# Kernel optimization log

Measured on AMD Instinct MI355X. Metric: run time of the kernel, lower is better.

The kernel has to match this reference:

```python
import jax, jax.numpy as jnp
import numpy as np

B, LT, D, N, H = 16, 512, 1024, 4096, 16
LN_EPS = 1e-5


def setup_inputs() -> dict:
    key = jax.random.key(0)
    ks = jax.random.split(key, 10)
    s = 0.02
    struct_token = jax.random.normal(ks[0], (N, D), dtype=jnp.float32)
    text_token = jax.random.normal(ks[1], (B, LT, D), dtype=jnp.float32)
    # contiguous, sorted segment ids: 256 struct tokens per batch element
    struct_batch = jnp.repeat(jnp.arange(B, dtype=jnp.int32), N // B)
    return {
        "struct_token": struct_token,
        "text_token": text_token,
        "in_proj_w": jax.random.normal(ks[2], (3 * D, D), dtype=jnp.float32) * s,
        "in_proj_b": jnp.zeros((3 * D,), jnp.float32),
        "attn_out_w": jax.random.normal(ks[3], (D, D), dtype=jnp.float32) * s,
        "attn_out_b": jnp.zeros((D,), jnp.float32),
        "ln_g": jnp.ones((D,), jnp.float32),
        "ln_b": jnp.zeros((D,), jnp.float32),
        "proj_w": jax.random.normal(ks[4], (D, D), dtype=jnp.float32) * s,
        "proj_b": jnp.zeros((D,), jnp.float32),
        "struct_batch": struct_batch,
        "L_max": N // B,
    }


def reference(struct_token, text_token, in_proj_w, in_proj_b, attn_out_w,
              attn_out_b, ln_g, ln_b, proj_w, proj_b, struct_batch, L_max):
    Bq = text_token.shape[0]
    Dm = struct_token.shape[-1]
    dh = Dm // H
    Ntok = struct_token.shape[0]

    # ---- ragged pad-pack (struct_batch is sorted/contiguous per segment) ----
    counts = jnp.bincount(struct_batch, length=Bq)                 # [B]
    starts = jnp.concatenate([jnp.zeros((1,), counts.dtype),
                              jnp.cumsum(counts)[:-1]])            # [B]
    pos = jnp.arange(Ntok) - starts[struct_batch]                  # [N] position in segment
    padded = jnp.zeros((Bq, L_max, Dm), struct_token.dtype)
    padded = padded.at[struct_batch, pos].set(struct_token)        # [B, Ls, D]

    # ---- nn.MultiheadAttention (batch_first): Q=padded, K=V=text ----
    wq, wk, wv = in_proj_w[:Dm], in_proj_w[Dm:2 * Dm], in_proj_w[2 * Dm:]
    bq, bk, bv = in_proj_b[:Dm], in_proj_b[Dm:2 * Dm], in_proj_b[2 * Dm:]
    q = (padded @ wq.T + bq).reshape(Bq, L_max, H, dh)
    k = (text_token @ wk.T + bk).reshape(Bq, -1, H, dh)
    v = (text_token @ wv.T + bv).reshape(Bq, -1, H, dh)
    scores = jnp.einsum('bqhd,bkhd->bhqk', q, k) / jnp.sqrt(jnp.float32(dh))
    attn = jax.nn.softmax(scores, axis=-1)
    ctx = jnp.einsum('bhqk,bkhd->bqhd', attn, v).reshape(Bq, L_max, Dm)
    fused = ctx @ attn_out_w.T + attn_out_b                        # [B, Ls, D]

    # ---- LayerNorm + output projection ----
    mu = fused.mean(-1, keepdims=True)
    var = fused.var(-1, keepdims=True)
    fused = (fused - mu) * jax.lax.rsqrt(var + LN_EPS) * ln_g + ln_b
    fused = fused @ proj_w.T + proj_b

    # ---- unpack valid tokens + scatter-mean over segments ----
    tok = fused[struct_batch, pos]                                 # [N, D]
    seg_sum = jax.ops.segment_sum(tok, struct_batch, num_segments=Bq)
    return seg_sum / jnp.maximum(counts, 1)[:, None].astype(seg_sum.dtype)
```

## Files before the change

kernel.cpp:

```cpp
#include <hip/hip_runtime.h>

constexpr int B  = 16;
constexpr int LT = 512;
constexpr int D  = 1024;
constexpr int N  = 4096;
constexpr int H  = 16;
constexpr int DH = D / H;
constexpr int LMAX = N / B;
constexpr float LN_EPS = 1e-5f;

typedef short  s16x8 __attribute__((ext_vector_type(8)));
typedef float  f32x4 __attribute__((ext_vector_type(4)));

__device__ __forceinline__ unsigned short f2bf(float x) {
    unsigned int u = __float_as_uint(x);
    unsigned int r = (u + 0x7fffu + ((u >> 16) & 1u)) >> 16;
    return (unsigned short)r;
}
__device__ __forceinline__ float bf2f(unsigned short u) {
    return __uint_as_float((unsigned int)u << 16);
}

__device__ __forceinline__ void load_lds16(const void* g, void* l) {
    __builtin_amdgcn_global_load_lds(
        (const __attribute__((address_space(1))) unsigned int*)g,
        (__attribute__((address_space(3))) unsigned int*)l, 16, 0, 0);
}

__global__ __launch_bounds__(256) void cast3_prep(
        const float* __restrict__ x0, unsigned short* __restrict__ y0, int n0,
        const float* __restrict__ x1, unsigned short* __restrict__ y1, int n1,
        const float* __restrict__ x2, unsigned short* __restrict__ y2, int n2,
        const int* __restrict__ sb, int* __restrict__ counts, int* __restrict__ starts) {
    __shared__ int s_counts[B];
    int t = threadIdx.x;
    if (blockIdx.x == 6144) {
        if (t < B) s_counts[t] = 0;
        __syncthreads();
        for (int i = t; i < N; i += 256) atomicAdd(&s_counts[sb[i]], 1);
        __syncthreads();
        if (t == 0) {
            int run = 0;
            for (int b = 0; b < B; b++) { starts[b] = run; run += s_counts[b]; }
        }
        if (t < B) counts[t] = s_counts[t];
        return;
    }
    long long i = (long long)(blockIdx.x * 256 + t) * 8;
    const float* x; unsigned short* y;
    if (i < n0)                { x = x0 + i; y = y0 + i; }
    else if (i < (long long)n0 + n1) { long long j = i - n0; x = x1 + j; y = y1 + j; }
    else if (i < (long long)n0 + n1 + n2) { long long j = i - n0 - n1; x = x2 + j; y = y2 + j; }
    else return;
    float4 a = *(const float4*)x;
    float4 b = *(const float4*)(x + 4);
    ushort4 o1, o2;
    o1.x = f2bf(a.x); o1.y = f2bf(a.y); o1.z = f2bf(a.z); o1.w = f2bf(a.w);
    o2.x = f2bf(b.x); o2.y = f2bf(b.y); o2.z = f2bf(b.z); o2.w = f2bf(b.w);
    *(ushort4*)y = o1;
    *(ushort4*)(y + 4) = o2;
}

__global__ void scatter_full(const float* __restrict__ st,
                             const int* __restrict__ counts,
                             const int* __restrict__ starts,
                             unsigned short* __restrict__ padded) {
    int p = blockIdx.x, b = blockIdx.y;
    int d = threadIdx.x * 4;
    size_t off = ((size_t)(b * LMAX + p)) * D + d;
    ushort4 o = {0, 0, 0, 0};
    if (p < counts[b]) {
        float4 v = *(const float4*)&st[(size_t)(starts[b] + p) * D + d];
        o.x = f2bf(v.x); o.y = f2bf(v.y); o.z = f2bf(v.z); o.w = f2bf(v.w);
    }
    *(ushort4*)&padded[off] = o;
}

template<typename Epi>
__device__ __forceinline__ void gemm256x128(const unsigned short* __restrict__ A,
                                            const unsigned short* __restrict__ W,
                                            int K, int kbeg, int kend, int m0, int n0,
                                            unsigned short* __restrict__ As,
                                            unsigned short* __restrict__ Bs,
                                            Epi&& epi) {
    const int tid  = threadIdx.x;
    const int lane = tid & 63;
    const int wid  = tid >> 6;
    const int wr   = wid >> 2;
    const int wc   = wid & 3;
    const int fm   = lane & 15;
    const int quad = lane >> 4;

    const int NK = (kend - kbeg) >> 6;

    f32x4 acc[8][2];
#pragma unroll
    for (int i = 0; i < 8; i++)
#pragma unroll
        for (int j = 0; j < 2; j++) acc[i][j] = (f32x4){0.f, 0.f, 0.f, 0.f};

    auto stage = [&](int s) {
        const int k0  = kbeg + (s << 6);
        const int buf = s - (s / 3) * 3;
        unsigned short* Ad = As + buf * 16384;
        unsigned short* Bd = Bs + buf * 8192;
#pragma unroll
        for (int r = 0; r < 4; r++) {
            int ci  = r * 512 + tid;
            int row = ci >> 3;
            int sg  = (ci & 7) ^ (row & 7);
            load_lds16(A + (size_t)(m0 + row) * K + k0 + sg * 8, Ad + ci * 8);
        }
#pragma unroll
        for (int r = 0; r < 2; r++) {
            int ci  = r * 512 + tid;
            int row = ci >> 3;
            int sg  = (ci & 7) ^ (row & 7);
            load_lds16(W + (size_t)(n0 + row) * K + k0 + sg * 8, Bd + ci * 8);
        }
    };

    stage(0);
    stage(1);

    for (int s = 0; s < NK; s++) {
        if (s + 1 < NK) asm volatile("s_waitcnt vmcnt(6)" ::: "memory");
        else            asm volatile("s_waitcnt vmcnt(0)" ::: "memory");
        __builtin_amdgcn_s_barrier();
        __builtin_amdgcn_sched_barrier(0);

        if (s + 2 < NK) stage(s + 2);

        const int buf = s - (s / 3) * 3;
        const unsigned short* Ab = As + buf * 16384;
        const unsigned short* Bb = Bs + buf * 8192;

        s16x8 bfr[2][2];
#pragma unroll
        for (int j = 0; j < 2; j++) {
            int row = wc * 32 + j * 16 + fm;
#pragma unroll
            for (int kk = 0; kk < 2; kk++) {
                int sl = (kk * 4 + quad) ^ (row & 7);
                bfr[j][kk] = *(const s16x8*)&Bb[row * 64 + sl * 8];
            }
        }

        s16x8 afr[4][2];
#pragma unroll
        for (int i = 0; i < 4; i++) {
            int row = wr * 128 + i * 16 + fm;
#pragma unroll
            for (int kk = 0; kk < 2; kk++) {
                int sl = (kk * 4 + quad) ^ (row & 7);
                afr[i][kk] = *(const s16x8*)&Ab[row * 64 + sl * 8];
            }
        }
        __builtin_amdgcn_s_setprio(1);
#pragma unroll
        for (int kk = 0; kk < 2; kk++)
#pragma unroll
            for (int i = 0; i < 4; i++)
#pragma unroll
                for (int j = 0; j < 2; j++)
                    acc[i][j] = __builtin_amdgcn_mfma_f32_16x16x32_bf16(afr[i][kk], bfr[j][kk], acc[i][j], 0, 0, 0);
        __builtin_amdgcn_s_setprio(0);

#pragma unroll
        for (int i = 0; i < 4; i++) {
            int row = wr * 128 + 64 + i * 16 + fm;
#pragma unroll
            for (int kk = 0; kk < 2; kk++) {
                int sl = (kk * 4 + quad) ^ (row & 7);
                afr[i][kk] = *(const s16x8*)&Ab[row * 64 + sl * 8];
            }
        }
        __builtin_amdgcn_s_setprio(1);
#pragma unroll
        for (int kk = 0; kk < 2; kk++)
#pragma unroll
            for (int i = 0; i < 4; i++)
#pragma unroll
                for (int j = 0; j < 2; j++)
                    acc[4 + i][j] = __builtin_amdgcn_mfma_f32_16x16x32_bf16(afr[i][kk], bfr[j][kk], acc[4 + i][j], 0, 0, 0);
        __builtin_amdgcn_s_setprio(0);
    }

    const int fr = quad * 4;
#pragma unroll
    for (int h = 0; h < 2; h++)
#pragma unroll
        for (int i = 0; i < 4; i++)
#pragma unroll
            for (int j = 0; j < 2; j++) {
                int row = m0 + wr * 128 + h * 64 + i * 16 + fr;
                int col = n0 + wc * 32 + j * 16 + fm;
#pragma unroll
                for (int r = 0; r < 4; r++)
                    epi(row + r, col, acc[h * 4 + i][j][r]);
            }
}

__global__ __launch_bounds__(512, 2) void qkv_fused(const unsigned short* __restrict__ padded,
                                                    const unsigned short* __restrict__ text,
                                                    const unsigned short* __restrict__ wqkv,
                                                    const float* __restrict__ bqkv,
                                                    unsigned short* __restrict__ qpack,
                                                    unsigned short* __restrict__ kpack,
                                                    unsigned short* __restrict__ vpack) {
    __shared__ __align__(16) unsigned short As[3 * 16384];
    __shared__ __align__(16) unsigned short Bs[3 * 8192];
    int orig = blockIdx.x;
    int id = (orig & 7) * 80 + (orig >> 3);
    if (id < 128) {
        int mt = id >> 3, nt = id & 7;
        gemm256x128(padded, wqkv, D, 0, D, mt * 256, nt * 128, As, Bs,
            [&](int mm, int col, float v) {
                float val = v + bqkv[col];
                int b = mm >> 8, q = mm & 255;
                int h = col >> 6, d = col & 63;
                qpack[(size_t)(b * H + h) * 16384 + (d >> 3) * 2048 + q * 8 + (d & 7)] = f2bf(val);
            });
    } else if (id < 384) {
        int f = id - 128;
        int mt = f >> 3, nt = f & 7;
        gemm256x128(text, wqkv + (size_t)D * D, D, 0, D, mt * 256, nt * 128, As, Bs,
            [&](int mm, int col, float v) {
                float val = v + bqkv[D + col];
                int b = mm >> 9, key = mm & 511;
                int h = col >> 6, d = col & 63;
                kpack[(size_t)(b * H + h) * 32768 + (d >> 3) * 4096 + key * 8 + (d & 7)] = f2bf(val);
            });
    } else {
        int f = id - 384;
        int mt = f >> 6, nt = f & 63;
        gemm256x128(wqkv + 2 * (size_t)D * D, text, D, 0, D, mt * 256, nt * 128, As, Bs,
            [&](int mm, int col, float v) {
                float val = v + bqkv[2 * D + mm];
                int h = mm >> 6, d = mm & 63;
                int b = col >> 9, key = col & 511;
                vpack[(size_t)(b * H + h) * 32768 + (key >> 3) * 512 + d * 8 + (key & 7)] = f2bf(val);
            });
    }
}

__global__ __launch_bounds__(512, 2) void gemm_bf2(const unsigned short* __restrict__ A,
                                                   const unsigned short* __restrict__ W,
                                                   unsigned short* __restrict__ C0,
                                                   unsigned short* __restrict__ C1,
                                                   int Nn, int K) {
    __shared__ __align__(16) unsigned short As[3 * 16384];
    __shared__ __align__(16) unsigned short Bs[3 * 8192];
    int orig = blockIdx.x;
    int id = (orig & 7) * 32 + (orig >> 3);
    int kh = id >> 7;
    int f  = id & 127;
    int mt = f >> 3, nt = f & 7;
    unsigned short* C = kh ? C1 : C0;
    gemm256x128(A, W, K, kh * 512, (kh + 1) * 512, mt * 256, nt * 128, As, Bs,
        [&](int mm, int col, float v) {
            C[(size_t)mm * Nn + col] = f2bf(v);
        });
}

constexpr int PKW = 72;

__global__ __launch_bounds__(512) void attn_mfma(const unsigned short* __restrict__ qpack,
                                                 const unsigned short* __restrict__ kpack,
                                                 const unsigned short* __restrict__ vpack,
                                                 unsigned short* __restrict__ ctx) {
    __shared__ __align__(16) unsigned short KV[16384];
    __shared__ __align__(16) unsigned short Ps[8 * 16 * PKW];

    const int tid = threadIdx.x;
    const int lane = tid & 63;
    const int wv = tid >> 6;
    const int fm = lane & 15;
    const int quad = lane >> 4;
    const int h = blockIdx.x, b = blockIdx.y, half = blockIdx.z;
    const int q0 = half * 128 + wv * 16;

    const unsigned short* qp = qpack + (size_t)(b * H + h) * 16384;
    const unsigned short* kp = kpack + (size_t)(b * H + h) * 32768;
    const unsigned short* vp = vpack + (size_t)(b * H + h) * 32768;

    const s16x8 aq0 = *(const s16x8*)&qp[quad * 2048 + (q0 + fm) * 8];
    const s16x8 aq1 = *(const s16x8*)&qp[(4 + quad) * 2048 + (q0 + fm) * 8];

    f32x4 sc[32];

    for (int kc = 0; kc < 2; kc++) {
        __syncthreads();
#pragma unroll
        for (int it = 0; it < 4; it++) {
            int f = it * 512 + tid;
            load_lds16(kp + (f >> 8) * 4096 + kc * 2048 + (f & 255) * 8, KV + f * 8);
        }
        __syncthreads();
#pragma unroll
        for (int t = 0; t < 16; t++) {
            s16x8 bk0 = *(const s16x8*)&KV[quad * 2048 + (t * 16 + fm) * 8];
            s16x8 bk1 = *(const s16x8*)&KV[(4 + quad) * 2048 + (t * 16 + fm) * 8];
            f32x4 a = (f32x4){0.f, 0.f, 0.f, 0.f};
            a = __builtin_amdgcn_mfma_f32_16x16x32_bf16(aq0, bk0, a, 0, 0, 0);
            a = __builtin_amdgcn_mfma_f32_16x16x32_bf16(aq1, bk1, a, 0, 0, 0);
            sc[kc * 16 + t] = a;
        }
    }

    const float scale = 0.125f;
    float mx[4], l[4], inv[4];
#pragma unroll
    for (int r = 0; r < 4; r++) {
        float m = sc[0][r];
#pragma unroll
        for (int t = 1; t < 32; t++) m = fmaxf(m, sc[t][r]);
        mx[r] = m;
    }
#pragma unroll
    for (int o = 1; o < 16; o <<= 1)
#pragma unroll
        for (int r = 0; r < 4; r++) mx[r] = fmaxf(mx[r], __shfl_xor(mx[r], o));
#pragma unroll
    for (int r = 0; r < 4; r++) l[r] = 0.f;
#pragma unroll
    for (int t = 0; t < 32; t++)
#pragma unroll
        for (int r = 0; r < 4; r++) {
            float e = __expf((sc[t][r] - mx[r]) * scale);
            sc[t][r] = e;
            l[r] += e;
        }
#pragma unroll
    for (int o = 1; o < 16; o <<= 1)
#pragma unroll
        for (int r = 0; r < 4; r++) l[r] += __shfl_xor(l[r], o);
#pragma unroll
    for (int r = 0; r < 4; r++) inv[r] = 1.f / l[r];

    f32x4 co[4];
#pragma unroll
    for (int n = 0; n < 4; n++) co[n] = (f32x4){0.f, 0.f, 0.f, 0.f};
    unsigned short* Pw = Ps + wv * (16 * PKW);

    for (int vc = 0; vc < 2; vc++) {
        __syncthreads();
#pragma unroll
        for (int it = 0; it < 4; it++) {
            int f = it * 512 + tid;
            load_lds16(vp + vc * 16384 + f * 8, KV + f * 8);
        }
        __syncthreads();
        for (int cs = 0; cs < 4; cs++) {
            int c = vc * 4 + cs;
#pragma unroll
            for (int tt = 0; tt < 4; tt++)
#pragma unroll
                for (int r = 0; r < 4; r++)
                    Pw[(quad * 4 + r) * PKW + tt * 16 + fm] = f2bf(sc[c * 4 + tt][r]);
#pragma unroll
            for (int s = 0; s < 2; s++) {
                s16x8 ap = *(const s16x8*)&Pw[fm * PKW + s * 32 + quad * 8];
#pragma unroll
                for (int n = 0; n < 4; n++) {
                    s16x8 bv = *(const s16x8*)&KV[(cs * 8 + s * 4 + quad) * 512 + (n * 16 + fm) * 8];
                    co[n] = __builtin_amdgcn_mfma_f32_16x16x32_bf16(ap, bv, co[n], 0, 0, 0);
                }
            }
        }
    }

    const size_t obase = (size_t)(b * LMAX + q0) * D + h * DH;
#pragma unroll
    for (int n = 0; n < 4; n++)
#pragma unroll
        for (int r = 0; r < 4; r++)
            ctx[obase + (size_t)(quad * 4 + r) * D + n * 16 + fm] = f2bf(co[n][r] * inv[r]);
}

__global__ __launch_bounds__(256) void lnmean_kernel(const unsigned short* __restrict__ f1a,
                                                     const unsigned short* __restrict__ f1b,
                                                     const float* __restrict__ bo,
                                                     const float* __restrict__ g,
                                                     const float* __restrict__ bb,
                                                     const int* __restrict__ counts,
                                                     float* __restrict__ msum) {
    int b = blockIdx.x;
    int t = threadIdx.x;
    int wv = t >> 6, lane = t & 63;
    int cnt = counts[b];
    int s0 = blockIdx.y * 32 + wv * 8;
    int s1 = min(cnt, s0 + 8);

    float4 gg[4], bv[4], bo4[4];
#pragma unroll
    for (int c = 0; c < 4; c++) {
        gg[c]  = *(const float4*)&g[c * 256 + lane * 4];
        bv[c]  = *(const float4*)&bb[c * 256 + lane * 4];
        bo4[c] = *(const float4*)&bo[c * 256 + lane * 4];
    }
    float4 acc[4];
#pragma unroll
    for (int c = 0; c < 4; c++) acc[c] = (float4){0.f, 0.f, 0.f, 0.f};

    for (int s = s0; s < s1; s++) {
        size_t rbase = ((size_t)(b * LMAX + s)) * D;
        float4 v[4];
        float sm = 0.f, ss = 0.f;
#pragma unroll
        for (int c = 0; c < 4; c++) {
            ushort4 ua = *(const ushort4*)&f1a[rbase + c * 256 + lane * 4];
            ushort4 ub = *(const ushort4*)&f1b[rbase + c * 256 + lane * 4];
            v[c].x = bf2f(ua.x) + bf2f(ub.x) + bo4[c].x;
            v[c].y = bf2f(ua.y) + bf2f(ub.y) + bo4[c].y;
            v[c].z = bf2f(ua.z) + bf2f(ub.z) + bo4[c].z;
            v[c].w = bf2f(ua.w) + bf2f(ub.w) + bo4[c].w;
            sm += v[c].x + v[c].y + v[c].z + v[c].w;
            ss += v[c].x * v[c].x + v[c].y * v[c].y + v[c].z * v[c].z + v[c].w * v[c].w;
        }
#pragma unroll
        for (int o = 32; o; o >>= 1) { sm += __shfl_xor(sm, o); ss += __shfl_xor(ss, o); }
        float mu = sm * (1.f / D);
        float var = ss * (1.f / D) - mu * mu;
        float r = rsqrtf(var + LN_EPS);
#pragma unroll
        for (int c = 0; c < 4; c++) {
            acc[c].x += (v[c].x - mu) * r * gg[c].x + bv[c].x;
            acc[c].y += (v[c].y - mu) * r * gg[c].y + bv[c].y;
            acc[c].z += (v[c].z - mu) * r * gg[c].z + bv[c].z;
            acc[c].w += (v[c].w - mu) * r * gg[c].w + bv[c].w;
        }
    }
    float inv = 1.f / (float)max(cnt, 1);
#pragma unroll
    for (int c = 0; c < 4; c++) {
        int base = b * D + c * 256 + lane * 4;
        atomicAdd(&msum[base + 0], acc[c].x * inv);
        atomicAdd(&msum[base + 1], acc[c].y * inv);
        atomicAdd(&msum[base + 2], acc[c].z * inv);
        atomicAdd(&msum[base + 3], acc[c].w * inv);
    }
}

__global__ __launch_bounds__(256) void tproj_kernel(const float* __restrict__ msum,
                                                    const float* __restrict__ W,
                                                    const float* __restrict__ bias,
                                                    float* __restrict__ out) {
    int lane = threadIdx.x & 63;
    int n = blockIdx.x * 4 + (threadIdx.x >> 6);
    float4 wr[4];
#pragma unroll
    for (int i = 0; i < 4; i++)
        wr[i] = *(const float4*)&W[(size_t)n * D + i * 256 + lane * 4];
    float bn = bias[n];
    for (int b = 0; b < B; b++) {
        float s = 0.f;
#pragma unroll
        for (int i = 0; i < 4; i++) {
            float4 m4 = *(const float4*)&msum[(size_t)b * D + i * 256 + lane * 4];
            s += m4.x * wr[i].x + m4.y * wr[i].y + m4.z * wr[i].z + m4.w * wr[i].w;
        }
#pragma unroll
        for (int o = 32; o; o >>= 1) s += __shfl_xor(s, o);
        if (lane == 0) out[(size_t)b * D + n] = s + bn;
    }
}

extern "C" void kernel_launch(void* const* d_in, const int* in_sizes, int n_in,
                              void* d_out, int out_size, void* d_ws, size_t ws_size,
                              hipStream_t stream) {
    const float* struct_token = (const float*)d_in[0];
    const float* text_token   = (const float*)d_in[1];
    const float* in_proj_w    = (const float*)d_in[2];
    const float* in_proj_b    = (const float*)d_in[3];
    const float* attn_out_w   = (const float*)d_in[4];
    const float* attn_out_b   = (const float*)d_in[5];
    const float* ln_g         = (const float*)d_in[6];
    const float* ln_b         = (const float*)d_in[7];
    const float* proj_w       = (const float*)d_in[8];
    const float* proj_b       = (const float*)d_in[9];
    const int*   sb           = (const int*)d_in[10];
    float* out = (float*)d_out;

    const size_t MQ  = (size_t)B * LMAX;
    const size_t MKV = (size_t)B * LT;

    char* p = (char*)d_ws;
    unsigned short* padded_b = (unsigned short*)p;  p += MQ * D * 2;
    unsigned short* text_b   = (unsigned short*)p;  p += MKV * D * 2;
    unsigned short* wqkv_b   = (unsigned short*)p;  p += (size_t)3 * D * D * 2;
    unsigned short* wattn_b  = (unsigned short*)p;  p += (size_t)D * D * 2;
    unsigned short* qpack    = (unsigned short*)p;  p += MQ * D * 2;
    unsigned short* kpack    = (unsigned short*)p;  p += MKV * D * 2;
    unsigned short* vpack    = (unsigned short*)p;  p += MKV * D * 2;
    unsigned short* ctx_b    = (unsigned short*)p;  p += MQ * D * 2;
    unsigned short* f1a      = (unsigned short*)p;  p += MQ * D * 2;
    unsigned short* f1b      = (unsigned short*)p;  p += MQ * D * 2;
    float* msum = (float*)p;  p += (size_t)B * D * 4;
    int* counts = (int*)p;  p += B * 4;
    int* starts = (int*)p;  p += B * 4;

    hipMemsetAsync(msum, 0, (size_t)B * D * 4, stream);

    cast3_prep<<<6145, 256, 0, stream>>>(
        text_token, text_b, (int)(MKV * D),
        in_proj_w,  wqkv_b, 3 * D * D,
        attn_out_w, wattn_b, D * D,
        sb, counts, starts);

    scatter_full<<<dim3(LMAX, B), 256, 0, stream>>>(struct_token, counts, starts, padded_b);

    qkv_fused<<<640, 512, 0, stream>>>(padded_b, text_b, wqkv_b, in_proj_b,
                                       qpack, kpack, vpack);

    attn_mfma<<<dim3(H, B, 2), 512, 0, stream>>>(qpack, kpack, vpack, ctx_b);

    gemm_bf2<<<256, 512, 0, stream>>>(ctx_b, wattn_b, f1a, f1b, D, D);

    lnmean_kernel<<<dim3(B, 8), 256, 0, stream>>>(f1a, f1b, attn_out_b, ln_g, ln_b, counts, msum);

    tproj_kernel<<<256, 256, 0, stream>>>(msum, proj_w, proj_b, out);
}
```

Measured before the change: 265.1 us.

## Rework GEMM wave layout to 4x2 with double-buffered LDS staging

```diff
diff --git a/kernel.cpp b/kernel.cpp
--- a/kernel.cpp
+++ b/kernel.cpp
@@ -77,33 +77,30 @@
 }
 
 template<typename Epi>
-__device__ __forceinline__ void gemm256x128(const unsigned short* __restrict__ A,
-                                            const unsigned short* __restrict__ W,
-                                            int K, int kbeg, int kend, int m0, int n0,
-                                            unsigned short* __restrict__ As,
-                                            unsigned short* __restrict__ Bs,
-                                            Epi&& epi) {
+__device__ __forceinline__ void gemm8ph(const unsigned short* __restrict__ A,
+                                        const unsigned short* __restrict__ W,
+                                        int K, int kbeg, int kend, int m0, int n0,
+                                        unsigned short* __restrict__ As,
+                                        unsigned short* __restrict__ Bs,
+                                        Epi&& epi) {
     const int tid  = threadIdx.x;
     const int lane = tid & 63;
     const int wid  = tid >> 6;
-    const int wr   = wid >> 2;
-    const int wc   = wid & 3;
+    const int wr   = wid >> 1;
+    const int wc   = wid & 1;
     const int fm   = lane & 15;
     const int quad = lane >> 4;
-
-    const int NK = (kend - kbeg) >> 6;
-
-    f32x4 acc[8][2];
-#pragma unroll
-    for (int i = 0; i < 8; i++)
-#pragma unroll
-        for (int j = 0; j < 2; j++) acc[i][j] = (f32x4){0.f, 0.f, 0.f, 0.f};
-
-    auto stage = [&](int s) {
-        const int k0  = kbeg + (s << 6);
-        const int buf = s - (s / 3) * 3;
-        unsigned short* Ad = As + buf * 16384;
-        unsigned short* Bd = Bs + buf * 8192;
+    const int NK   = (kend - kbeg) >> 6;
+
+    f32x4 acc[4][4];
+#pragma unroll
+    for (int i = 0; i < 4; i++)
+#pragma unroll
+        for (int j = 0; j < 4; j++) acc[i][j] = (f32x4){0.f, 0.f, 0.f, 0.f};
+
+    auto stageA = [&](int s) {
+        const int k0 = kbeg + (s << 6);
+        unsigned short* Ad = As + (s & 1) * 16384;
 #pragma unroll
         for (int r = 0; r < 4; r++) {
             int ci  = r * 512 + tid;
@@ -111,6 +108,10 @@
             int sg  = (ci & 7) ^ (row & 7);
             load_lds16(A + (size_t)(m0 + row) * K + k0 + sg * 8, Ad + ci * 8);
         }
+    };
+    auto stageB = [&](int s) {
+        const int k0 = kbeg + (s << 6);
+        unsigned short* Bd = Bs + (s & 1) * 8192;
 #pragma unroll
         for (int r = 0; r < 2; r++) {
             int ci  = r * 512 + tid;
@@ -120,42 +121,42 @@
         }
     };
 
-    stage(0);
-    stage(1);
+    stageA(0);
+    stageB(0);
 
     for (int s = 0; s < NK; s++) {
+        const unsigned short* Ab = As + (s & 1) * 16384;
+        const unsigned short* Bb = Bs + (s & 1) * 8192;
+
+        __builtin_amdgcn_s_barrier();
+        __builtin_amdgcn_sched_barrier(0);
+        if (s + 1 < NK) { stageA(s + 1); stageB(s + 1); }
         if (s + 1 < NK) asm volatile("s_waitcnt vmcnt(6)" ::: "memory");
         else            asm volatile("s_waitcnt vmcnt(0)" ::: "memory");
         __builtin_amdgcn_s_barrier();
         __builtin_amdgcn_sched_barrier(0);
 
-        if (s + 2 < NK) stage(s + 2);
-
-        const int buf = s - (s / 3) * 3;
-        const unsigned short* Ab = As + buf * 16384;
-        const unsigned short* Bb = Bs + buf * 8192;
-
-        s16x8 bfr[2][2];
-#pragma unroll
-        for (int j = 0; j < 2; j++) {
-            int row = wc * 32 + j * 16 + fm;
+        s16x8 af[4][2], bf0[2][2];
+#pragma unroll
+        for (int i = 0; i < 4; i++) {
+            int row = wr * 64 + i * 16 + fm;
 #pragma unroll
             for (int kk = 0; kk < 2; kk++) {
                 int sl = (kk * 4 + quad) ^ (row & 7);
-                bfr[j][kk] = *(const s16x8*)&Bb[row * 64 + sl * 8];
+                af[i][kk] = *(const s16x8*)&Ab[row * 64 + sl * 8];
             }
         }
-
-        s16x8 afr[4][2];
-#pragma unroll
-        for (int i = 0; i < 4; i++) {
-            int row = wr * 128 + i * 16 + fm;
+#pragma unroll
+        for (int j = 0; j < 2; j++) {
+            int row = wc * 64 + j * 16 + fm;
 #pragma unroll
             for (int kk = 0; kk < 2; kk++) {
                 int sl = (kk * 4 + quad) ^ (row & 7);
-                afr[i][kk] = *(const s16x8*)&Ab[row * 64 + sl * 8];
+                bf0[j][kk] = *(const s16x8*)&Bb[row * 64 + sl * 8];
             }
         }
+        asm volatile("s_waitcnt lgkmcnt(0)" ::: "memory");
+        __builtin_amdgcn_sched_barrier(0);
         __builtin_amdgcn_s_setprio(1);
 #pragma unroll
         for (int kk = 0; kk < 2; kk++)
@@ -163,18 +164,21 @@
             for (int i = 0; i < 4; i++)
 #pragma unroll
                 for (int j = 0; j < 2; j++)
-                    acc[i][j] = __builtin_amdgcn_mfma_f32_16x16x32_bf16(afr[i][kk], bfr[j][kk], acc[i][j], 0, 0, 0);
+                    acc[i][j] = __builtin_amdgcn_mfma_f32_16x16x32_bf16(af[i][kk], bf0[j][kk], acc[i][j], 0, 0, 0);
         __builtin_amdgcn_s_setprio(0);
 
-#pragma unroll
-        for (int i = 0; i < 4; i++) {
-            int row = wr * 128 + 64 + i * 16 + fm;
+        s16x8 bf1[2][2];
+#pragma unroll
+        for (int j = 0; j < 2; j++) {
+            int row = wc * 64 + (2 + j) * 16 + fm;
 #pragma unroll
             for (int kk = 0; kk < 2; kk++) {
                 int sl = (kk * 4 + quad) ^ (row & 7);
-                afr[i][kk] = *(const s16x8*)&Ab[row * 64 + sl * 8];
+                bf1[j][kk] = *(const s16x8*)&Bb[row * 64 + sl * 8];
             }
         }
+        asm volatile("s_waitcnt lgkmcnt(0)" ::: "memory");
+        __builtin_amdgcn_sched_barrier(0);
         __builtin_amdgcn_s_setprio(1);
 #pragma unroll
         for (int kk = 0; kk < 2; kk++)
@@ -182,23 +186,21 @@
             for (int i = 0; i < 4; i++)
 #pragma unroll
                 for (int j = 0; j < 2; j++)
-                    acc[4 + i][j] = __builtin_amdgcn_mfma_f32_16x16x32_bf16(afr[i][kk], bfr[j][kk], acc[4 + i][j], 0, 0, 0);
+                    acc[i][2 + j] = __builtin_amdgcn_mfma_f32_16x16x32_bf16(af[i][kk], bf1[j][kk], acc[i][2 + j], 0, 0, 0);
         __builtin_amdgcn_s_setprio(0);
     }
 
     const int fr = quad * 4;
 #pragma unroll
-    for (int h = 0; h < 2; h++)
-#pragma unroll
-        for (int i = 0; i < 4; i++)
-#pragma unroll
-            for (int j = 0; j < 2; j++) {
-                int row = m0 + wr * 128 + h * 64 + i * 16 + fr;
-                int col = n0 + wc * 32 + j * 16 + fm;
-#pragma unroll
-                for (int r = 0; r < 4; r++)
-                    epi(row + r, col, acc[h * 4 + i][j][r]);
-            }
+    for (int i = 0; i < 4; i++)
+#pragma unroll
+        for (int j = 0; j < 4; j++) {
+            int row = m0 + wr * 64 + i * 16 + fr;
+            int col = n0 + wc * 64 + j * 16 + fm;
+#pragma unroll
+            for (int r = 0; r < 4; r++)
+                epi(row + r, col, acc[i][j][r]);
+        }
 }
 
 __global__ __launch_bounds__(512, 2) void qkv_fused(const unsigned short* __restrict__ padded,
@@ -208,13 +210,13 @@
                                                     unsigned short* __restrict__ qpack,
                                                     unsigned short* __restrict__ kpack,
                                                     unsigned short* __restrict__ vpack) {
-    __shared__ __align__(16) unsigned short As[3 * 16384];
-    __shared__ __align__(16) unsigned short Bs[3 * 8192];
+    __shared__ __align__(16) unsigned short As[2 * 16384];
+    __shared__ __align__(16) unsigned short Bs[2 * 8192];
     int orig = blockIdx.x;
     int id = (orig & 7) * 80 + (orig >> 3);
     if (id < 128) {
         int mt = id >> 3, nt = id & 7;
-        gemm256x128(padded, wqkv, D, 0, D, mt * 256, nt * 128, As, Bs,
+        gemm8ph(padded, wqkv, D, 0, D, mt * 256, nt * 128, As, Bs,
             [&](int mm, int col, float v) {
                 float val = v + bqkv[col];
                 int b = mm >> 8, q = mm & 255;
@@ -224,7 +226,7 @@
     } else if (id < 384) {
         int f = id - 128;
         int mt = f >> 3, nt = f & 7;
-        gemm256x128(text, wqkv + (size_t)D * D, D, 0, D, mt * 256, nt * 128, As, Bs,
+        gemm8ph(text, wqkv + (size_t)D * D, D, 0, D, mt * 256, nt * 128, As, Bs,
             [&](int mm, int col, float v) {
                 float val = v + bqkv[D + col];
                 int b = mm >> 9, key = mm & 511;
@@ -234,7 +236,7 @@
     } else {
         int f = id - 384;
         int mt = f >> 6, nt = f & 63;
-        gemm256x128(wqkv + 2 * (size_t)D * D, text, D, 0, D, mt * 256, nt * 128, As, Bs,
+        gemm8ph(wqkv + 2 * (size_t)D * D, text, D, 0, D, mt * 256, nt * 128, As, Bs,
             [&](int mm, int col, float v) {
                 float val = v + bqkv[2 * D + mm];
                 int h = mm >> 6, d = mm & 63;
@@ -249,15 +251,15 @@
                                                    unsigned short* __restrict__ C0,
                                                    unsigned short* __restrict__ C1,
                                                    int Nn, int K) {
-    __shared__ __align__(16) unsigned short As[3 * 16384];
-    __shared__ __align__(16) unsigned short Bs[3 * 8192];
+    __shared__ __align__(16) unsigned short As[2 * 16384];
+    __shared__ __align__(16) unsigned short Bs[2 * 8192];
     int orig = blockIdx.x;
     int id = (orig & 7) * 32 + (orig >> 3);
     int kh = id >> 7;
     int f  = id & 127;
     int mt = f >> 3, nt = f & 7;
     unsigned short* C = kh ? C1 : C0;
-    gemm256x128(A, W, K, kh * 512, (kh + 1) * 512, mt * 256, nt * 128, As, Bs,
+    gemm8ph(A, W, K, kh * 512, (kh + 1) * 512, mt * 256, nt * 128, As, Bs,
         [&](int mm, int col, float v) {
             C[(size_t)mm * Nn + col] = f2bf(v);
         });
```

Result: no change. 267.7 us (+1.0%).
